# Kernel optimization log

Measured on AMD Instinct MI355X. Metric: run time of the kernel, lower is better.

## Reference

```python
import jax, jax.numpy as jnp
import numpy as np

N, P, C = 8, 256, 128


def setup_inputs() -> dict:
    key = jax.random.key(0)
    ks = jax.random.split(key, 16)
    s = lambda k, shape, fan_in: jax.random.normal(k, shape, jnp.float32) / np.sqrt(fan_in)
    return {
        "x": jax.random.normal(ks[0], (N, P, C), jnp.float32),
        "pos": jax.random.normal(ks[1], (N, P, P, 2), jnp.float32),
        # projections (no bias), stored (in, out)
        "Wq": s(ks[2], (C, C), C),
        "Wk": s(ks[3], (C, C), C),
        "Wv": s(ks[4], (C, C), C),
        # qk_mlp: Linear(C,C) -> ReLU -> Linear(C,1)
        "W1": s(ks[5], (C, C), C),
        "b1": jnp.zeros((C,), jnp.float32),
        "W2": s(ks[6], (C, 1), C),
        "b2": jnp.zeros((1,), jnp.float32),
        # pos_mlp: Linear(2,C) -> ReLU -> Linear(C,C)
        "Wp1": s(ks[7], (2, C), 2),
        "bp1": jnp.zeros((C,), jnp.float32),
        "Wp2": s(ks[8], (C, C), C),
        "bp2": jnp.zeros((C,), jnp.float32),
    }


def reference(x, pos, Wq, Wk, Wv, W1, b1, W2, b2, Wp1, bp1, Wp2, bp2):
    # x: [N,P,C], pos: [N,P,P,2]
    q = x @ Wq  # [N,P,C]
    k = x @ Wk
    v = x @ Wv
    pos_emb = jax.nn.relu(pos @ Wp1 + bp1) @ Wp2 + bp2  # [N,P,P,C]
    # diff[n,a,b,:] = q[n,b] - k[n,a] + pos_emb[n,a,b]
    diff = q[:, None, :, :] - k[:, :, None, :] + pos_emb  # [N,P,P,C]
    att = (jax.nn.relu(diff @ W1 + b1) @ W2 + b2)[..., 0]  # [N,P,P]
    att = jax.nn.softmax(att, axis=-1)
    # out[n,a] = sum_b att[n,a,b] * v[n,b]
    fuse = jnp.einsum("nab,nbc->nac", att, v)
    return x + fuse
```

## Files before the change

kernel.cpp:

```cpp
#include <hip/hip_runtime.h>
#include <hip/hip_bf16.h>

#define NB 8
#define PP 256
#define CC 128
#define XS 132

typedef __bf16 bf16x8 __attribute__((ext_vector_type(8)));
typedef float float4v __attribute__((ext_vector_type(4)));

__device__ __forceinline__ float bf2f(unsigned short u) {
    union { unsigned int i; float f; } x; x.i = ((unsigned int)u) << 16; return x.f;
}
__device__ __forceinline__ unsigned short f2bf(float f) {
    union { float f; unsigned int i; } x; x.f = f;
    unsigned int r = x.i + 0x7fffu + ((x.i >> 16) & 1u);
    return (unsigned short)(r >> 16);
}
__device__ __forceinline__ unsigned int pk2(float a, float b) {
    return (unsigned int)f2bf(a) | ((unsigned int)f2bf(b) << 16);
}

__global__ __launch_bounds__(256) void stage1_kernel(
    const float* __restrict__ x, const float* __restrict__ Wq,
    const float* __restrict__ Wk, const float* __restrict__ Wv,
    const float* __restrict__ W1, const float* __restrict__ b1,
    const float* __restrict__ bp2, const float* __restrict__ Wp2,
    unsigned short* __restrict__ qwtb, float* __restrict__ kw,
    float* __restrict__ v, unsigned short* __restrict__ W21f,
    float* __restrict__ bvec)
{
    __shared__ __attribute__((aligned(16))) float Wbuf[CC * CC];
    __shared__ __attribute__((aligned(16))) float xs[32 * XS];
    __shared__ __attribute__((aligned(16))) float tmp[32 * XS];
    const int t = threadIdx.x, bx = blockIdx.x;

    if (bx == 196) {
        if (t < 128) {
            float s = b1[t];
#pragma unroll 8
            for (int c = 0; c < CC; ++c) s = fmaf(bp2[c], W1[c * CC + t], s);
            bvec[t] = s;
        }
        return;
    }

    const int tc = t & 31, tr = t >> 5;
    const int j0 = tc * 4, r0 = tr * 4;

    if (bx < 192) {
        const int kind = bx >> 6;
        const int row0 = (bx & 63) * 32;
        const float* Wsrc = (kind == 0) ? Wq : (kind == 1) ? Wk : Wv;
#pragma unroll 4
        for (int i = 0; i < 16; ++i)
            ((float4*)Wbuf)[i * 256 + t] = ((const float4*)Wsrc)[i * 256 + t];
#pragma unroll
        for (int i = 0; i < 4; ++i) {
            int idx = i * 256 + t; int r = idx >> 5, c4 = idx & 31;
            *(float4*)&xs[r * XS + c4 * 4] =
                ((const float4*)(x + (size_t)(row0 + r) * CC))[c4];
        }
        __syncthreads();
        float4 acc[4];
#pragma unroll
        for (int i = 0; i < 4; ++i) acc[i] = make_float4(0.f, 0.f, 0.f, 0.f);
#pragma unroll 2
        for (int c4 = 0; c4 < 32; ++c4) {
            float4 xv0 = *(const float4*)&xs[(r0 + 0) * XS + c4 * 4];
            float4 xv1 = *(const float4*)&xs[(r0 + 1) * XS + c4 * 4];
            float4 xv2 = *(const float4*)&xs[(r0 + 2) * XS + c4 * 4];
            float4 xv3 = *(const float4*)&xs[(r0 + 3) * XS + c4 * 4];
            const float xr[4][4] = {{xv0.x, xv0.y, xv0.z, xv0.w},
                                    {xv1.x, xv1.y, xv1.z, xv1.w},
                                    {xv2.x, xv2.y, xv2.z, xv2.w},
                                    {xv3.x, xv3.y, xv3.z, xv3.w}};
#pragma unroll
            for (int cc = 0; cc < 4; ++cc) {
                float4 w4 = *(const float4*)&Wbuf[(c4 * 4 + cc) * CC + j0];
#pragma unroll
                for (int i = 0; i < 4; ++i) {
                    acc[i].x = fmaf(xr[i][cc], w4.x, acc[i].x);
                    acc[i].y = fmaf(xr[i][cc], w4.y, acc[i].y);
                    acc[i].z = fmaf(xr[i][cc], w4.z, acc[i].z);
                    acc[i].w = fmaf(xr[i][cc], w4.w, acc[i].w);
                }
            }
        }
        if (kind == 2) {
#pragma unroll
            for (int i = 0; i < 4; ++i)
                *(float4*)&v[(size_t)(row0 + r0 + i) * CC + j0] = acc[i];
            return;
        }
#pragma unroll
        for (int i = 0; i < 4; ++i)
            *(float4*)&tmp[(r0 + i) * XS + j0] = acc[i];
        __syncthreads();
#pragma unroll 4
        for (int i = 0; i < 16; ++i)
            ((float4*)Wbuf)[i * 256 + t] = ((const float4*)W1)[i * 256 + t];
        __syncthreads();
        float4 acc2[4];
#pragma unroll
        for (int i = 0; i < 4; ++i) acc2[i] = make_float4(0.f, 0.f, 0.f, 0.f);
#pragma unroll 2
        for (int c4 = 0; c4 < 32; ++c4) {
            float4 xv0 = *(const float4*)&tmp[(r0 + 0) * XS + c4 * 4];
            float4 xv1 = *(const float4*)&tmp[(r0 + 1) * XS + c4 * 4];
            float4 xv2 = *(const float4*)&tmp[(r0 + 2) * XS + c4 * 4];
            float4 xv3 = *(const float4*)&tmp[(r0 + 3) * XS + c4 * 4];
            const float xr[4][4] = {{xv0.x, xv0.y, xv0.z, xv0.w},
                                    {xv1.x, xv1.y, xv1.z, xv1.w},
                                    {xv2.x, xv2.y, xv2.z, xv2.w},
                                    {xv3.x, xv3.y, xv3.z, xv3.w}};
#pragma unroll
            for (int cc = 0; cc < 4; ++cc) {
                float4 w4 = *(const float4*)&Wbuf[(c4 * 4 + cc) * CC + j0];
#pragma unroll
                for (int i = 0; i < 4; ++i) {
                    acc2[i].x = fmaf(xr[i][cc], w4.x, acc2[i].x);
                    acc2[i].y = fmaf(xr[i][cc], w4.y, acc2[i].y);
                    acc2[i].z = fmaf(xr[i][cc], w4.z, acc2[i].z);
                    acc2[i].w = fmaf(xr[i][cc], w4.w, acc2[i].w);
                }
            }
        }
        if (kind == 0) {
            int n = row0 >> 8, b0 = row0 & 255;
            const float a2[4][4] = {{acc2[0].x, acc2[0].y, acc2[0].z, acc2[0].w},
                                    {acc2[1].x, acc2[1].y, acc2[1].z, acc2[1].w},
                                    {acc2[2].x, acc2[2].y, acc2[2].z, acc2[2].w},
                                    {acc2[3].x, acc2[3].y, acc2[3].z, acc2[3].w}};
#pragma unroll
            for (int jj = 0; jj < 4; ++jj) {
                ushort4 pk;
                pk.x = f2bf(a2[0][jj]); pk.y = f2bf(a2[1][jj]);
                pk.z = f2bf(a2[2][jj]); pk.w = f2bf(a2[3][jj]);
                *(ushort4*)(qwtb + (size_t)(n * CC + j0 + jj) * PP + b0 + r0) = pk;
            }
        } else {
#pragma unroll
            for (int i = 0; i < 4; ++i)
                *(float4*)&kw[(size_t)(row0 + r0 + i) * CC + j0] = acc2[i];
        }
    } else {
        const int row0 = (bx - 192) * 32;
#pragma unroll 4
        for (int i = 0; i < 16; ++i)
            ((float4*)Wbuf)[i * 256 + t] = ((const float4*)W1)[i * 256 + t];
#pragma unroll
        for (int i = 0; i < 4; ++i) {
            int idx = i * 256 + t; int r = idx >> 5, c4 = idx & 31;
            *(float4*)&xs[r * XS + c4 * 4] =
                ((const float4*)(Wp2 + (size_t)(row0 + r) * CC))[c4];
        }
        __syncthreads();
        float4 acc[4];
#pragma unroll
        for (int i = 0; i < 4; ++i) acc[i] = make_float4(0.f, 0.f, 0.f, 0.f);
#pragma unroll 2
        for (int c4 = 0; c4 < 32; ++c4) {
            float4 xv0 = *(const float4*)&xs[(r0 + 0) * XS + c4 * 4];
            float4 xv1 = *(const float4*)&xs[(r0 + 1) * XS + c4 * 4];
            float4 xv2 = *(const float4*)&xs[(r0 + 2) * XS + c4 * 4];
            float4 xv3 = *(const float4*)&xs[(r0 + 3) * XS + c4 * 4];
            const float xr[4][4] = {{xv0.x, xv0.y, xv0.z, xv0.w},
                                    {xv1.x, xv1.y, xv1.z, xv1.w},
                                    {xv2.x, xv2.y, xv2.z, xv2.w},
                                    {xv3.x, xv3.y, xv3.z, xv3.w}};
#pragma unroll
            for (int cc = 0; cc < 4; ++cc) {
                float4 w4 = *(const float4*)&Wbuf[(c4 * 4 + cc) * CC + j0];
#pragma unroll
                for (int i = 0; i < 4; ++i) {
                    acc[i].x = fmaf(xr[i][cc], w4.x, acc[i].x);
                    acc[i].y = fmaf(xr[i][cc], w4.y, acc[i].y);
                    acc[i].z = fmaf(xr[i][cc], w4.z, acc[i].z);
                    acc[i].w = fmaf(xr[i][cc], w4.w, acc[i].w);
                }
            }
        }
        const float a4[4][4] = {{acc[0].x, acc[0].y, acc[0].z, acc[0].w},
                                {acc[1].x, acc[1].y, acc[1].z, acc[1].w},
                                {acc[2].x, acc[2].y, acc[2].z, acc[2].w},
                                {acc[3].x, acc[3].y, acc[3].z, acc[3].w}};
#pragma unroll
        for (int i = 0; i < 4; ++i)
#pragma unroll
            for (int jj = 0; jj < 4; ++jj) {
                int k = row0 + r0 + i, j = j0 + jj;
                int kk = k >> 5, qd = (k >> 3) & 3, e = k & 7;
                int jt = j >> 4, ln = j & 15, lane = qd * 16 + ln;
                W21f[(((kk * 8 + jt) * 64) + lane) * 8 + e] = f2bf(a4[i][jj]);
            }
    }
}

__global__ __launch_bounds__(256, 3) void attn_kernel(
    const float* __restrict__ x, const float* __restrict__ pos,
    const float* __restrict__ Wp1, const float* __restrict__ bp1,
    const float* __restrict__ W2, const float* __restrict__ b2,
    const unsigned short* __restrict__ W21f, const float* __restrict__ bvec,
    const unsigned short* __restrict__ qwtb, const float* __restrict__ kw,
    const float* __restrict__ v, float* __restrict__ out)
{
    __shared__ __attribute__((aligned(16))) unsigned short Bs[128 * 128];
    __shared__ float p0s[PP], p1s[PP];
    __shared__ float wa[CC], wb[CC], bpv[CC];
    __shared__ float logits[PP];
    __shared__ float red[8];
    __shared__ float avp[8 * 128];

    const int t = threadIdx.x;
    const int n = blockIdx.x >> 8, a = blockIdx.x & 255;
    const int lane = t & 63, wv = t >> 6;
    const int ln = lane & 15, quad = lane >> 4;

    if (t < CC) {
        wa[t]  = Wp1[t];
        wb[t]  = Wp1[CC + t];
        bpv[t] = bp1[t];
    }
    {
        const float2* pr = (const float2*)(pos + (size_t)(n * PP + a) * PP * 2);
        float2 pp = pr[t];
        p0s[t] = pp.x;
        p1s[t] = pp.y;
    }
    {
        const uint4* src = (const uint4*)W21f;
        uint4* dst = (uint4*)Bs;
#pragma unroll
        for (int i = 0; i < 8; ++i) dst[i * 256 + t] = src[i * 256 + t];
    }
    const float b2f = b2[0];

    float w2v[8], kbv[8];
    {
        const float* kwrow = kw + (size_t)(n * PP + a) * CC;
#pragma unroll
        for (int nt = 0; nt < 8; ++nt) {
            int j = nt * 16 + ln;
            w2v[nt] = W2[j];
            kbv[nt] = bvec[j] - kwrow[j];
        }
    }
    __syncthreads();

#pragma unroll 1
    for (int chunk = 0; chunk < 4; ++chunk) {
        const int rbase = chunk * 64 + wv * 16;
        const float P0 = p0s[rbase + ln];
        const float P1 = p1s[rbase + ln];

        ushort4 qv4[8];
#pragma unroll
        for (int nt = 0; nt < 8; ++nt)
            qv4[nt] = *(const ushort4*)(qwtb + (size_t)(n * CC + nt * 16 + ln) * PP
                                        + rbase + quad * 4);

        float4v acc[8];
#pragma unroll
        for (int j = 0; j < 8; ++j) acc[j] = (float4v)0.f;

#pragma unroll 1
        for (int kk = 0; kk < 4; ++kk) {
            const int ko = kk * 32 + quad * 8;
            float4 a0 = *(const float4*)&wa[ko],  a1 = *(const float4*)&wa[ko + 4];
            float4 c0 = *(const float4*)&wb[ko],  c1 = *(const float4*)&wb[ko + 4];
            float4 d0 = *(const float4*)&bpv[ko], d1 = *(const float4*)&bpv[ko + 4];
            float h0 = fmaxf(fmaf(P0, a0.x, fmaf(P1, c0.x, d0.x)), 0.f);
            float h1 = fmaxf(fmaf(P0, a0.y, fmaf(P1, c0.y, d0.y)), 0.f);
            float h2 = fmaxf(fmaf(P0, a0.z, fmaf(P1, c0.z, d0.z)), 0.f);
            float h3 = fmaxf(fmaf(P0, a0.w, fmaf(P1, c0.w, d0.w)), 0.f);
            float h4 = fmaxf(fmaf(P0, a1.x, fmaf(P1, c1.x, d1.x)), 0.f);
            float h5 = fmaxf(fmaf(P0, a1.y, fmaf(P1, c1.y, d1.y)), 0.f);
            float h6 = fmaxf(fmaf(P0, a1.z, fmaf(P1, c1.z, d1.z)), 0.f);
            float h7 = fmaxf(fmaf(P0, a1.w, fmaf(P1, c1.w, d1.w)), 0.f);
            union { bf16x8 v8; unsigned int u[4]; } cv;
            cv.u[0] = pk2(h0, h1); cv.u[1] = pk2(h2, h3);
            cv.u[2] = pk2(h4, h5); cv.u[3] = pk2(h6, h7);
            bf16x8 af = cv.v8;
#pragma unroll
            for (int j = 0; j < 8; ++j) {
                bf16x8 bfr = *(const bf16x8*)(Bs + (((kk * 8 + j) * 64) + lane) * 8);
                acc[j] = __builtin_amdgcn_mfma_f32_16x16x32_bf16(af, bfr, acc[j], 0, 0, 0);
            }
        }

        float s0 = 0.f, s1 = 0.f, s2 = 0.f, s3 = 0.f;
#pragma unroll
        for (int nt = 0; nt < 8; ++nt) {
            float kb = kbv[nt], w2 = w2v[nt];
            s0 = fmaf(fmaxf(acc[nt][0] + bf2f(qv4[nt].x) + kb, 0.f), w2, s0);
            s1 = fmaf(fmaxf(acc[nt][1] + bf2f(qv4[nt].y) + kb, 0.f), w2, s1);
            s2 = fmaf(fmaxf(acc[nt][2] + bf2f(qv4[nt].z) + kb, 0.f), w2, s2);
            s3 = fmaf(fmaxf(acc[nt][3] + bf2f(qv4[nt].w) + kb, 0.f), w2, s3);
        }
        float sr[4] = {s0, s1, s2, s3};
#pragma unroll
        for (int r = 0; r < 4; ++r) {
            float s = sr[r];
            s += __shfl_xor(s, 1);
            s += __shfl_xor(s, 2);
            s += __shfl_xor(s, 4);
            s += __shfl_xor(s, 8);
            if (ln == 0) logits[rbase + quad * 4 + r] = s + b2f;
        }
    }
    __syncthreads();

    float lv = logits[t];
    float wm = lv;
#pragma unroll
    for (int d = 1; d < 64; d <<= 1) wm = fmaxf(wm, __shfl_xor(wm, d));
    if (lane == 0) red[wv] = wm;
    __syncthreads();
    float m = fmaxf(fmaxf(red[0], red[1]), fmaxf(red[2], red[3]));
    float e = __expf(lv - m);
    float es = e;
#pragma unroll
    for (int d = 1; d < 64; d <<= 1) es += __shfl_xor(es, d);
    if (lane == 0) red[4 + wv] = es;
    __syncthreads();
    float denom = red[4] + red[5] + red[6] + red[7];
    logits[t] = e / denom;
    __syncthreads();

    {
        int c4 = (t & 31) * 4, bg = t >> 5;
        const float* vp = v + (size_t)(n * PP + bg * 32) * CC + c4;
        float4 av = make_float4(0.f, 0.f, 0.f, 0.f);
#pragma unroll 4
        for (int b = 0; b < 32; ++b) {
            float w = logits[bg * 32 + b];
            float4 vv = *(const float4*)(vp + (size_t)b * CC);
            av.x = fmaf(w, vv.x, av.x); av.y = fmaf(w, vv.y, av.y);
            av.z = fmaf(w, vv.z, av.z); av.w = fmaf(w, vv.w, av.w);
        }
        *(float4*)&avp[bg * 128 + c4] = av;
    }
    __syncthreads();
    if (t < 128) {
        int oidx = (n * PP + a) * CC + t;
        float s = x[oidx];
#pragma unroll
        for (int g = 0; g < 8; ++g) s += avp[g * 128 + t];
        out[oidx] = s;
    }
}

extern "C" void kernel_launch(void* const* d_in, const int* in_sizes, int n_in,
                              void* d_out, int out_size, void* d_ws, size_t ws_size,
                              hipStream_t stream) {
    const float* x   = (const float*)d_in[0];
    const float* pos = (const float*)d_in[1];
    const float* Wq  = (const float*)d_in[2];
    const float* Wk  = (const float*)d_in[3];
    const float* Wv  = (const float*)d_in[4];
    const float* W1  = (const float*)d_in[5];
    const float* b1  = (const float*)d_in[6];
    const float* W2  = (const float*)d_in[7];
    const float* b2  = (const float*)d_in[8];
    const float* Wp1 = (const float*)d_in[9];
    const float* bp1 = (const float*)d_in[10];
    const float* Wp2 = (const float*)d_in[11];
    const float* bp2 = (const float*)d_in[12];
    float* out = (float*)d_out;

    float* ws   = (float*)d_ws;
    float* bvec = ws;
    float* kw   = bvec + 128;
    float* v    = kw + 262144;
    unsigned short* qwtb = (unsigned short*)(v + 262144);
    unsigned short* W21f = qwtb + 262144;

    stage1_kernel<<<197, 256, 0, stream>>>(x, Wq, Wk, Wv, W1, b1, bp2, Wp2,
                                           qwtb, kw, v, W21f, bvec);
    attn_kernel<<<NB * PP, 256, 0, stream>>>(x, pos, Wp1, bp1, W2, b2,
                                             W21f, bvec, qwtb, kw, v, out);
}
```

Measured before the change: 142.2 us.

## Shrink shared memory via bf16 weights and aliased pool to raise occupancy

```diff
diff --git a/kernel.cpp b/kernel.cpp
--- a/kernel.cpp
+++ b/kernel.cpp
@@ -17,11 +17,19 @@
     unsigned int r = x.i + 0x7fffu + ((x.i >> 16) & 1u);
     return (unsigned short)(r >> 16);
 }
-__device__ __forceinline__ unsigned int pk2(float a, float b) {
-    return (unsigned int)f2bf(a) | ((unsigned int)f2bf(b) << 16);
-}
-
-__global__ __launch_bounds__(256) void stage1_kernel(
+__device__ __forceinline__ unsigned int pkbf2(float a, float b) {
+    union { __hip_bfloat162 b2; unsigned int u; } cv;
+    cv.b2 = __float22bfloat162_rn(make_float2(a, b));
+    return cv.u;
+}
+__device__ __forceinline__ float lo2f(unsigned int u) {
+    union { unsigned int i; float f; } x; x.i = u << 16; return x.f;
+}
+__device__ __forceinline__ float hi2f(unsigned int u) {
+    union { unsigned int i; float f; } x; x.i = u & 0xffff0000u; return x.f;
+}
+
+__global__ __launch_bounds__(256, 2) void stage1_kernel(
     const float* __restrict__ x, const float* __restrict__ Wq,
     const float* __restrict__ Wk, const float* __restrict__ Wv,
     const float* __restrict__ W1, const float* __restrict__ b1,
@@ -30,7 +38,7 @@
     float* __restrict__ v, unsigned short* __restrict__ W21f,
     float* __restrict__ bvec)
 {
-    __shared__ __attribute__((aligned(16))) float Wbuf[CC * CC];
+    __shared__ __attribute__((aligned(16))) unsigned int WbufU[CC * CC / 2];
     __shared__ __attribute__((aligned(16))) float xs[32 * XS];
     __shared__ __attribute__((aligned(16))) float tmp[32 * XS];
     const int t = threadIdx.x, bx = blockIdx.x;
@@ -47,14 +55,18 @@
 
     const int tc = t & 31, tr = t >> 5;
     const int j0 = tc * 4, r0 = tr * 4;
+    const int jd = tc * 2;
 
     if (bx < 192) {
         const int kind = bx >> 6;
         const int row0 = (bx & 63) * 32;
         const float* Wsrc = (kind == 0) ? Wq : (kind == 1) ? Wk : Wv;
 #pragma unroll 4
-        for (int i = 0; i < 16; ++i)
-            ((float4*)Wbuf)[i * 256 + t] = ((const float4*)Wsrc)[i * 256 + t];
+        for (int i = 0; i < 16; ++i) {
+            float4 w = ((const float4*)Wsrc)[i * 256 + t];
+            uint2 p; p.x = pkbf2(w.x, w.y); p.y = pkbf2(w.z, w.w);
+            ((uint2*)WbufU)[i * 256 + t] = p;
+        }
 #pragma unroll
         for (int i = 0; i < 4; ++i) {
             int idx = i * 256 + t; int r = idx >> 5, c4 = idx & 31;
@@ -77,13 +89,15 @@
                                     {xv3.x, xv3.y, xv3.z, xv3.w}};
 #pragma unroll
             for (int cc = 0; cc < 4; ++cc) {
-                float4 w4 = *(const float4*)&Wbuf[(c4 * 4 + cc) * CC + j0];
+                uint2 wp = *(const uint2*)&WbufU[(c4 * 4 + cc) * 64 + jd];
+                float w0 = lo2f(wp.x), w1 = hi2f(wp.x);
+                float w2 = lo2f(wp.y), w3 = hi2f(wp.y);
 #pragma unroll
                 for (int i = 0; i < 4; ++i) {
-                    acc[i].x = fmaf(xr[i][cc], w4.x, acc[i].x);
-                    acc[i].y = fmaf(xr[i][cc], w4.y, acc[i].y);
-                    acc[i].z = fmaf(xr[i][cc], w4.z, acc[i].z);
-                    acc[i].w = fmaf(xr[i][cc], w4.w, acc[i].w);
+                    acc[i].x = fmaf(xr[i][cc], w0, acc[i].x);
+                    acc[i].y = fmaf(xr[i][cc], w1, acc[i].y);
+                    acc[i].z = fmaf(xr[i][cc], w2, acc[i].z);
+                    acc[i].w = fmaf(xr[i][cc], w3, acc[i].w);
                 }
             }
         }
@@ -98,8 +112,11 @@
             *(float4*)&tmp[(r0 + i) * XS + j0] = acc[i];
         __syncthreads();
 #pragma unroll 4
-        for (int i = 0; i < 16; ++i)
-            ((float4*)Wbuf)[i * 256 + t] = ((const float4*)W1)[i * 256 + t];
+        for (int i = 0; i < 16; ++i) {
+            float4 w = ((const float4*)W1)[i * 256 + t];
+            uint2 p; p.x = pkbf2(w.x, w.y); p.y = pkbf2(w.z, w.w);
+            ((uint2*)WbufU)[i * 256 + t] = p;
+        }
         __syncthreads();
         float4 acc2[4];
 #pragma unroll
@@ -116,13 +133,15 @@
                                     {xv3.x, xv3.y, xv3.z, xv3.w}};
 #pragma unroll
             for (int cc = 0; cc < 4; ++cc) {
-                float4 w4 = *(const float4*)&Wbuf[(c4 * 4 + cc) * CC + j0];
+                uint2 wp = *(const uint2*)&WbufU[(c4 * 4 + cc) * 64 + jd];
+                float w0 = lo2f(wp.x), w1 = hi2f(wp.x);
+                float w2 = lo2f(wp.y), w3 = hi2f(wp.y);
 #pragma unroll
                 for (int i = 0; i < 4; ++i) {
-                    acc2[i].x = fmaf(xr[i][cc], w4.x, acc2[i].x);
-                    acc2[i].y = fmaf(xr[i][cc], w4.y, acc2[i].y);
-                    acc2[i].z = fmaf(xr[i][cc], w4.z, acc2[i].z);
-                    acc2[i].w = fmaf(xr[i][cc], w4.w, acc2[i].w);
+                    acc2[i].x = fmaf(xr[i][cc], w0, acc2[i].x);
+                    acc2[i].y = fmaf(xr[i][cc], w1, acc2[i].y);
+                    acc2[i].z = fmaf(xr[i][cc], w2, acc2[i].z);
+                    acc2[i].w = fmaf(xr[i][cc], w3, acc2[i].w);
                 }
             }
         }
@@ -147,8 +166,11 @@
     } else {
         const int row0 = (bx - 192) * 32;
 #pragma unroll 4
-        for (int i = 0; i < 16; ++i)
-            ((float4*)Wbuf)[i * 256 + t] = ((const float4*)W1)[i * 256 + t];
+        for (int i = 0; i < 16; ++i) {
+            float4 w = ((const float4*)W1)[i * 256 + t];
+            uint2 p; p.x = pkbf2(w.x, w.y); p.y = pkbf2(w.z, w.w);
+            ((uint2*)WbufU)[i * 256 + t] = p;
+        }
 #pragma unroll
         for (int i = 0; i < 4; ++i) {
             int idx = i * 256 + t; int r = idx >> 5, c4 = idx & 31;
@@ -171,13 +193,15 @@
                                     {xv3.x, xv3.y, xv3.z, xv3.w}};
 #pragma unroll
             for (int cc = 0; cc < 4; ++cc) {
-                float4 w4 = *(const float4*)&Wbuf[(c4 * 4 + cc) * CC + j0];
+                uint2 wp = *(const uint2*)&WbufU[(c4 * 4 + cc) * 64 + jd];
+                float w0 = lo2f(wp.x), w1 = hi2f(wp.x);
+                float w2 = lo2f(wp.y), w3 = hi2f(wp.y);
 #pragma unroll
                 for (int i = 0; i < 4; ++i) {
-                    acc[i].x = fmaf(xr[i][cc], w4.x, acc[i].x);
-                    acc[i].y = fmaf(xr[i][cc], w4.y, acc[i].y);
-                    acc[i].z = fmaf(xr[i][cc], w4.z, acc[i].z);
-                    acc[i].w = fmaf(xr[i][cc], w4.w, acc[i].w);
+                    acc[i].x = fmaf(xr[i][cc], w0, acc[i].x);
+                    acc[i].y = fmaf(xr[i][cc], w1, acc[i].y);
+                    acc[i].z = fmaf(xr[i][cc], w2, acc[i].z);
+                    acc[i].w = fmaf(xr[i][cc], w3, acc[i].w);
                 }
             }
         }
@@ -197,7 +221,7 @@
     }
 }
 
-__global__ __launch_bounds__(256, 3) void attn_kernel(
+__global__ __launch_bounds__(256, 4) void attn_kernel(
     const float* __restrict__ x, const float* __restrict__ pos,
     const float* __restrict__ Wp1, const float* __restrict__ bp1,
     const float* __restrict__ W2, const float* __restrict__ b2,
@@ -206,11 +230,16 @@
     const float* __restrict__ v, float* __restrict__ out)
 {
     __shared__ __attribute__((aligned(16))) unsigned short Bs[128 * 128];
-    __shared__ float p0s[PP], p1s[PP];
-    __shared__ float wa[CC], wb[CC], bpv[CC];
+    __shared__ __attribute__((aligned(16))) float pool[1024];
     __shared__ float logits[PP];
     __shared__ float red[8];
-    __shared__ float avp[8 * 128];
+
+    float* const wa   = pool;
+    float* const wb   = pool + 128;
+    float* const bpv  = pool + 256;
+    float* const p0s  = pool + 384;
+    float* const p1s  = pool + 640;
+    float* const avp  = pool;
 
     const int t = threadIdx.x;
     const int n = blockIdx.x >> 8, a = blockIdx.x & 255;
@@ -279,8 +308,8 @@
             float h6 = fmaxf(fmaf(P0, a1.z, fmaf(P1, c1.z, d1.z)), 0.f);
             float h7 = fmaxf(fmaf(P0, a1.w, fmaf(P1, c1.w, d1.w)), 0.f);
             union { bf16x8 v8; unsigned int u[4]; } cv;
-            cv.u[0] = pk2(h0, h1); cv.u[1] = pk2(h2, h3);
-            cv.u[2] = pk2(h4, h5); cv.u[3] = pk2(h6, h7);
+            cv.u[0] = pkbf2(h0, h1); cv.u[1] = pkbf2(h2, h3);
+            cv.u[2] = pkbf2(h4, h5); cv.u[3] = pkbf2(h6, h7);
             bf16x8 af = cv.v8;
 #pragma unroll
             for (int j = 0; j < 8; ++j) {
```

Measured after the change: 141.5 us, median of 2. About the same (-0.5%).
